# Optimization experiments

Hardware: AMD Instinct MI355X
Metric: run time of the kernel (lower is better)

Reference implementation:

```python
import jax, jax.numpy as jnp
jax.config.update("jax_enable_x64", True)
import numpy as np

B = 1_000_000

def _basis_and_weights():
    # 7 Lie-algebra generators of the homography group (4x4), as in the torch module
    E = np.zeros((7, 4, 4), dtype=np.float64)
    E[0, 0, 3] = 1.0   # x translation
    E[1, 1, 3] = 1.0   # y translation
    E[2, 2, 3] = 1.0   # z translation
    E[3, 1, 2] = -1.0; E[3, 2, 1] = 1.0   # yz rotation generator
    E[4, 0, 2] = 1.0;  E[4, 2, 0] = -1.0  # xz rotation generator
    E[5, 0, 1] = -1.0; E[5, 1, 0] = 1.0   # xy rotation generator
    E[6, 0, 0] = 1.0;  E[6, 1, 1] = -1.0  # xy stretch generator
    w = np.ones((7,), dtype=np.float64)   # all *_weight init kwargs = 1.0
    return jnp.asarray(E), jnp.asarray(w)


def setup_inputs() -> dict:
    key = jax.random.key(0)
    lie_vectors = jax.random.normal(key, (B, 7), dtype=jnp.float32)
    return {"lie_vectors": lie_vectors}


def reference(lie_vectors):
    elements, weights = _basis_and_weights()
    # weighted sum of basis elements: (B,7) x (7,4,4) -> (B,4,4), in float64 (dtype_cast_to)
    A = jnp.einsum("bk,kij->bij", lie_vectors.astype(jnp.float64) * weights, elements)
    # batched 4x4 matrix exponential
    T = jax.vmap(jax.scipy.linalg.expm)(A)
    # homogeneous normalization by the (3,3) entry
    T = T / T[:, 3:4, 3:4]
    return T.astype(jnp.float32)  # dtype_out
```

## Files before the change

### kernel.cpp

```cpp
#include <hip/hip_runtime.h>

#define BLOCK 256

__global__ __launch_bounds__(BLOCK) void lie_expm_kernel(
    const float* __restrict__ in, float* __restrict__ out, int B)
{
    __shared__ float sh[BLOCK * 16];
    const int tid = threadIdx.x;
    const long long blockBase = (long long)blockIdx.x * BLOCK;

    {
        const long long gbase = blockBase * 7;
        int valid = B - (int)blockBase;
        if (valid > BLOCK) valid = BLOCK;
        const int limit = valid * 7;
        #pragma unroll
        for (int j = 0; j < 7; ++j) {
            const int i = j * BLOCK + tid;
            sh[i] = (i < limit) ? in[gbase + i] : 0.0f;
        }
    }
    __syncthreads();

    const float v0 = sh[tid * 7 + 0];
    const float v1 = sh[tid * 7 + 1];
    const float v2 = sh[tid * 7 + 2];
    const float v3 = sh[tid * 7 + 3];
    const float v4 = sh[tid * 7 + 4];
    const float v5 = sh[tid * 7 + 5];
    const float v6 = sh[tid * 7 + 6];

    const float sc = 0.015625f;
    float X[3][4] = {
        {  v6 * sc, -v5 * sc,  v4 * sc, v0 * sc },
        {  v5 * sc, -v6 * sc, -v3 * sc, v1 * sc },
        { -v4 * sc,  v3 * sc,     0.0f, v2 * sc }
    };

    float A2[3][4];
    #pragma unroll
    for (int i = 0; i < 3; i++) {
        #pragma unroll
        for (int c = 0; c < 4; c++) {
            float acc = X[i][0] * X[0][c];
            acc = fmaf(X[i][1], X[1][c], acc);
            acc = fmaf(X[i][2], X[2][c], acc);
            A2[i][c] = acc;
        }
    }

    const float c120 = 1.0f / 120.0f;
    const float c10  = 0.1f;
    float W[3][4];
    #pragma unroll
    for (int i = 0; i < 3; i++)
        #pragma unroll
        for (int c = 0; c < 4; c++)
            W[i][c] = fmaf(A2[i][c], c120, (i == c) ? 0.5f : 0.0f);

    float Nm[3][4], Dm[3][4];
    #pragma unroll
    for (int i = 0; i < 3; i++) {
        #pragma unroll
        for (int c = 0; c < 4; c++) {
            float u = (c == 3) ? 0.5f * X[i][3] : 0.0f;
            u = fmaf(X[i][0], W[0][c], u);
            u = fmaf(X[i][1], W[1][c], u);
            u = fmaf(X[i][2], W[2][c], u);
            float v = fmaf(A2[i][c], c10, (i == c) ? 1.0f : 0.0f);
            Nm[i][c] = v + u;
            Dm[i][c] = v - u;
        }
    }

    const float d00 = Dm[0][0], d01 = Dm[0][1], d02 = Dm[0][2];
    const float d10 = Dm[1][0], d11 = Dm[1][1], d12 = Dm[1][2];
    const float d20 = Dm[2][0], d21 = Dm[2][1], d22 = Dm[2][2];
    const float a00 = fmaf(d11, d22, -d12 * d21);
    const float a01 = fmaf(d02, d21, -d01 * d22);
    const float a02 = fmaf(d01, d12, -d02 * d11);
    const float a10 = fmaf(d12, d20, -d10 * d22);
    const float a11 = fmaf(d00, d22, -d02 * d20);
    const float a12 = fmaf(d02, d10, -d00 * d12);
    const float a20 = fmaf(d10, d21, -d11 * d20);
    const float a21 = fmaf(d01, d20, -d00 * d21);
    const float a22 = fmaf(d00, d11, -d01 * d10);
    float det = d00 * a00 + d01 * a10 + d02 * a20;
    float r = __builtin_amdgcn_rcpf(det);
    r = r * fmaf(-det, r, 2.0f);
    const float i00 = a00 * r, i01 = a01 * r, i02 = a02 * r;
    const float i10 = a10 * r, i11 = a11 * r, i12 = a12 * r;
    const float i20 = a20 * r, i21 = a21 * r, i22 = a22 * r;

    float P[3][4];
    float rhs0 = Nm[0][3] - Dm[0][3], rhs1 = Nm[1][3] - Dm[1][3], rhs2 = Nm[2][3] - Dm[2][3];
    #pragma unroll
    for (int c = 0; c < 3; c++) {
        P[0][c] = i00 * Nm[0][c] + i01 * Nm[1][c] + i02 * Nm[2][c];
        P[1][c] = i10 * Nm[0][c] + i11 * Nm[1][c] + i12 * Nm[2][c];
        P[2][c] = i20 * Nm[0][c] + i21 * Nm[1][c] + i22 * Nm[2][c];
    }
    P[0][3] = i00 * rhs0 + i01 * rhs1 + i02 * rhs2;
    P[1][3] = i10 * rhs0 + i11 * rhs1 + i12 * rhs2;
    P[2][3] = i20 * rhs0 + i21 * rhs1 + i22 * rhs2;

    #pragma unroll
    for (int q = 0; q < 6; q++) {
        float T[3][4];
        #pragma unroll
        for (int i = 0; i < 3; i++) {
            #pragma unroll
            for (int c = 0; c < 4; c++) {
                float acc = (c == 3) ? P[i][3] : 0.0f;
                acc = fmaf(P[i][0], P[0][c], acc);
                acc = fmaf(P[i][1], P[1][c], acc);
                acc = fmaf(P[i][2], P[2][c], acc);
                T[i][c] = acc;
            }
        }
        #pragma unroll
        for (int i = 0; i < 3; i++)
            #pragma unroll
            for (int c = 0; c < 4; c++)
                P[i][c] = T[i][c];
    }

    __syncthreads();

    {
        const int rot = (tid >> 1) & 15;
        float row3[4] = { 0.0f, 0.0f, 0.0f, 1.0f };
        #pragma unroll
        for (int k = 0; k < 16; k++) {
            const int i = k >> 2, c = k & 3;
            const float val = (i < 3) ? P[i][c] : row3[c];
            sh[tid * 16 + ((k + rot) & 15)] = val;
        }
    }
    __syncthreads();

    {
        const long long gbase16 = blockBase * 16;
        long long remll = (long long)B * 16 - gbase16;
        const int rem = (remll > BLOCK * 16) ? (BLOCK * 16) : (int)remll;
        #pragma unroll
        for (int it = 0; it < 16; it++) {
            const int f = it * BLOCK + tid;
            const int row = f >> 4, col = f & 15;
            const float val = sh[row * 16 + ((col + ((row >> 1) & 15)) & 15)];
            if (f < rem) out[gbase16 + f] = val;
        }
    }
}

extern "C" void kernel_launch(void* const* d_in, const int* in_sizes, int n_in,
                              void* d_out, int out_size, void* d_ws, size_t ws_size,
                              hipStream_t stream) {
    const float* in = (const float*)d_in[0];
    float* out = (float*)d_out;
    const int B = in_sizes[0] / 7;
    const int grid = (B + BLOCK - 1) / BLOCK;
    lie_expm_kernel<<<grid, BLOCK, 0, stream>>>(in, out, B);
}
```

Baseline: 95.20 us.

## Vectorize global I/O with float4 and adapt squaring count per wavefront norm

Input loads and output stores are rewritten to use float4 accesses through shared memory, with a quad-granular rotation to limit bank conflicts. The fixed scaling by 1/64 with six squarings is replaced by a per-wavefront scaling exponent taken from the max row-sum norm, reduced across lanes by shuffles and made uniform via readfirstlane. Wavefronts whose inputs have small norm then do fewer squarings, cutting ALU work in a kernel that is close to memory-bound. The risk is accuracy, since the Padé degree stays fixed while the scaling now depends on the norm, and large inputs are capped at eight squarings.

Result: faster. 89.29 us (-6.2%).

```diff
diff --git a/kernel.cpp b/kernel.cpp
--- a/kernel.cpp
+++ b/kernel.cpp
@@ -10,14 +10,23 @@
     const long long blockBase = (long long)blockIdx.x * BLOCK;
 
     {
-        const long long gbase = blockBase * 7;
         int valid = B - (int)blockBase;
         if (valid > BLOCK) valid = BLOCK;
         const int limit = valid * 7;
+        const int nf4 = limit >> 2;
+        const float4* in4 = (const float4*)(in + blockBase * 7);
+        float4* sh4 = (float4*)sh;
         #pragma unroll
-        for (int j = 0; j < 7; ++j) {
-            const int i = j * BLOCK + tid;
-            sh[i] = (i < limit) ? in[gbase + i] : 0.0f;
+        for (int it = 0; it < 2; ++it) {
+            const int idx = it * BLOCK + tid;
+            if (idx < nf4) sh4[idx] = in4[idx];
+        }
+        const int remf = limit & 3;
+        if (tid < remf) sh[nf4 * 4 + tid] = in[blockBase * 7 + nf4 * 4 + tid];
+        #pragma unroll
+        for (int it = 0; it < 7; ++it) {
+            const int i = it * BLOCK + tid;
+            if (i >= limit && i < BLOCK * 7) sh[i] = 0.0f;
         }
     }
     __syncthreads();
@@ -30,12 +39,29 @@
     const float v5 = sh[tid * 7 + 5];
     const float v6 = sh[tid * 7 + 6];
 
-    const float sc = 0.015625f;
     float X[3][4] = {
-        {  v6 * sc, -v5 * sc,  v4 * sc, v0 * sc },
-        {  v5 * sc, -v6 * sc, -v3 * sc, v1 * sc },
-        { -v4 * sc,  v3 * sc,     0.0f, v2 * sc }
+        {  v6, -v5,  v4, v0 },
+        {  v5, -v6, -v3, v1 },
+        { -v4,  v3, 0.0f, v2 }
     };
+
+    float n0 = fabsf(X[0][0]) + fabsf(X[0][1]) + fabsf(X[0][2]) + fabsf(X[0][3]);
+    float n1 = fabsf(X[1][0]) + fabsf(X[1][1]) + fabsf(X[1][2]) + fabsf(X[1][3]);
+    float n2 = fabsf(X[2][0]) + fabsf(X[2][1]) + fabsf(X[2][2]) + fabsf(X[2][3]);
+    float nrm = fmaxf(n0, fmaxf(n1, n2));
+    #pragma unroll
+    for (int off = 32; off >= 1; off >>= 1)
+        nrm = fmaxf(nrm, __shfl_xor(nrm, off, 64));
+    int e = (int)((__float_as_uint(nrm) >> 23) & 0xFFu) - 126;
+    int s = min(max(e + 1, 0), 8);
+    s = __builtin_amdgcn_readfirstlane(s);
+    const float sc = __uint_as_float((unsigned)(127 - s) << 23);
+
+    #pragma unroll
+    for (int i = 0; i < 3; i++)
+        #pragma unroll
+        for (int c = 0; c < 4; c++)
+            X[i][c] *= sc;
 
     float A2[3][4];
     #pragma unroll
@@ -104,8 +130,7 @@
     P[1][3] = i10 * rhs0 + i11 * rhs1 + i12 * rhs2;
     P[2][3] = i20 * rhs0 + i21 * rhs1 + i22 * rhs2;
 
-    #pragma unroll
-    for (int q = 0; q < 6; q++) {
+    for (int q = 0; q < s; q++) {
         float T[3][4];
         #pragma unroll
         for (int i = 0; i < 3; i++) {
@@ -126,29 +151,30 @@
     }
 
     __syncthreads();
-
     {
-        const int rot = (tid >> 1) & 15;
-        float row3[4] = { 0.0f, 0.0f, 0.0f, 1.0f };
+        float4* sh4 = (float4*)sh;
+        const int rot = (tid >> 1) & 3;
         #pragma unroll
-        for (int k = 0; k < 16; k++) {
-            const int i = k >> 2, c = k & 3;
-            const float val = (i < 3) ? P[i][c] : row3[c];
-            sh[tid * 16 + ((k + rot) & 15)] = val;
+        for (int i = 0; i < 4; i++) {
+            const int qp = (i + rot) & 3;
+            float4 q;
+            if (i < 3) q = make_float4(P[i][0], P[i][1], P[i][2], P[i][3]);
+            else       q = make_float4(0.0f, 0.0f, 0.0f, 1.0f);
+            sh4[tid * 4 + qp] = q;
         }
     }
     __syncthreads();
-
     {
-        const long long gbase16 = blockBase * 16;
-        long long remll = (long long)B * 16 - gbase16;
-        const int rem = (remll > BLOCK * 16) ? (BLOCK * 16) : (int)remll;
+        const float4* sh4 = (const float4*)sh;
+        float4* out4 = (float4*)(out + blockBase * 16);
+        long long vq = ((long long)B - blockBase) * 4;
+        const int validquads = (vq > BLOCK * 4) ? (BLOCK * 4) : (int)vq;
         #pragma unroll
-        for (int it = 0; it < 16; it++) {
-            const int f = it * BLOCK + tid;
-            const int row = f >> 4, col = f & 15;
-            const float val = sh[row * 16 + ((col + ((row >> 1) & 15)) & 15)];
-            if (f < rem) out[gbase16 + f] = val;
+        for (int it = 0; it < 4; it++) {
+            const int g = it * BLOCK + tid;
+            const int row = g >> 2, k = g & 3;
+            const float4 val = sh4[(row << 2) | ((k + ((row >> 1) & 3)) & 3)];
+            if (g < validquads) out4[g] = val;
         }
     }
 }
```
